# Performance work log

Measured on AMD Instinct MI355X. Metric: run time of the kernel, lower is better.

The kernel has to match this reference:

```python
import jax, jax.numpy as jnp
import numpy as np

H = 12           # num_heads
D_MODEL = 768
SCALE = (D_MODEL // H) ** -0.5  # qk_scale default: head_dim**-0.5


def _attn_mask(q, k, v, mask):
    # sim: (b, i, j); mask broadcast over query dim (mask.unsqueeze(1) in torch)
    sim = jnp.einsum('bid,bjd->bij', q, k) + mask[:, None, :]
    a = jax.nn.softmax(sim, axis=-1)
    return jnp.einsum('bij,bjd->bid', a, v)


def setup_inputs() -> dict:
    key = jax.random.key(0)
    k0, k1, k2, k3 = jax.random.split(key, 4)
    B, F, n, D = 16, 8, 196, 768
    N = 1 + F * n  # cls + frames*patches = 1569
    x = jax.random.normal(k0, (B, N, D), jnp.float32)
    x_mask = jax.random.normal(k1, (B, N), jnp.float32)  # additive attention mask
    Wqkv = jax.random.normal(k2, (3 * D, D), jnp.float32) * (D ** -0.5)
    Wproj = jax.random.normal(k3, (D, D), jnp.float32) * (D ** -0.5)
    bproj = jnp.zeros((D,), jnp.float32)
    return {"x": x, "x_mask": x_mask, "Wqkv": Wqkv, "Wproj": Wproj,
            "bproj": bproj, "f": F}


def reference(x, x_mask, Wqkv, Wproj, bproj, f):
    B, N, D = x.shape
    h = H
    d = D // h
    # qkv projection (qkv_bias=False), split into q,k,v
    qkv = x @ Wqkv.T                       # (B, N, 3D)
    q, k, v = jnp.split(qkv, 3, axis=-1)

    def to_heads(t):  # 'b n (h d) -> (b h) n d'
        return t.reshape(B, N, h, d).transpose(0, 2, 1, 3).reshape(B * h, N, d)

    q, k, v = map(to_heads, (q, k, v))
    mask = jnp.repeat(x_mask, h, axis=0)   # repeat_interleave over heads: (B*h, N)

    q = q * SCALE
    cls_q, q_ = q[:, :1], q[:, 1:]
    cls_k, k_ = k[:, :1], k[:, 1:]
    cls_v, v_ = v[:, :1], v[:, 1:]
    cls_mask, mask_ = mask[:, :1], mask[:, 1:]

    # cls token attends to everything
    cls_out = _attn_mask(cls_q, k, v, mask)            # (B*h, 1, d)

    # spatial attention: 'b (f n) d -> (b f) n d'
    n = (N - 1) // f
    q_ = q_.reshape(B * h * f, n, d)
    k_ = k_.reshape(B * h * f, n, d)
    v_ = v_.reshape(B * h * f, n, d)
    mask_ = mask_.reshape(B * h * f, n)

    # prepend cls k/v/mask to every frame group (r = f)
    cls_k = jnp.repeat(cls_k, f, axis=0)               # (B*h*f, 1, d)
    cls_v = jnp.repeat(cls_v, f, axis=0)
    cls_m = jnp.repeat(cls_mask, f, axis=0)            # (B*h*f, 1)
    k_ = jnp.concatenate([cls_k, k_], axis=1)          # (B*h*f, n+1, d)
    v_ = jnp.concatenate([cls_v, v_], axis=1)
    m2 = jnp.concatenate([cls_m, mask_], axis=1)       # (B*h*f, n+1)

    out = _attn_mask(q_, k_, v_, m2)                   # (B*h*f, n, d)
    out = out.reshape(B * h, f * n, d)                 # '(b f) n d -> b (f n) d'
    out = jnp.concatenate([cls_out, out], axis=1)      # (B*h, N, d)
    out = out.reshape(B, h, N, d).transpose(0, 2, 1, 3).reshape(B, N, D)
    return out @ Wproj.T + bproj
```

## Files before the change

### kernel.cpp

```cpp
#include <hip/hip_runtime.h>
#include <hip/hip_bf16.h>
#include <stdint.h>

#define Hh 12
#define Dm 768
#define Bb 16
#define Nt 1569
#define Ff 8
#define NC 196
#define BH 192
#define Mr 25104
#define CPW 224
#define VTW (8*CPW)
#define PLD 232
#define CLD 132

typedef __attribute__((ext_vector_type(8))) short bf16x8;
typedef __attribute__((ext_vector_type(4))) float f32x4;

typedef const __attribute__((address_space(1))) uint32_t guint;
typedef __attribute__((address_space(3))) uint32_t luint;

static __device__ __forceinline__ float bf2f(unsigned short u) {
  union { unsigned int i; float f; } v; v.i = ((unsigned int)u) << 16; return v.f;
}
static __device__ __forceinline__ unsigned short f2bf(float f) {
  __hip_bfloat16 h = __float2bfloat16(f);
  return __builtin_bit_cast(unsigned short, h);
}

__global__ void cast3_k(const float4* __restrict__ s0, ushort4* __restrict__ d0, int n0,
                        const float4* __restrict__ s1, ushort4* __restrict__ d1, int n1,
                        const float4* __restrict__ s2, ushort4* __restrict__ d2, int n2) {
  int nTot = n0 + n1 + n2;
  for (int i = blockIdx.x * blockDim.x + threadIdx.x; i < nTot; i += gridDim.x * blockDim.x) {
    const float4* s; ushort4* d; int off;
    if (i < n0) { s = s0; d = d0; off = i; }
    else if (i < n0 + n1) { s = s1; d = d1; off = i - n0; }
    else { s = s2; d = d2; off = i - n0 - n1; }
    float4 f = s[off];
    ushort4 u;
    u.x = f2bf(f.x); u.y = f2bf(f.y); u.z = f2bf(f.z); u.w = f2bf(f.w);
    d[off] = u;
  }
}

template<int MODE>
__global__ __launch_bounds__(256) void gemm_k(
    const __hip_bfloat16* __restrict__ A,
    const __hip_bfloat16* __restrict__ W,
    int M, int K,
    __hip_bfloat16* __restrict__ qh, __hip_bfloat16* __restrict__ kh,
    __hip_bfloat16* __restrict__ vT, __hip_bfloat16* __restrict__ vcls,
    const float* __restrict__ bias, float* __restrict__ outp)
{
  __shared__ __align__(16) unsigned short shmem[128 * CLD];
  unsigned short* ls0 = shmem;
  unsigned short* ls1 = shmem + 4096;
  unsigned short* ls2 = shmem + 8192;
  unsigned short* ls3 = shmem + 12288;

  const int tid = threadIdx.x;
  const int lane = tid & 63, wid = tid >> 6;
  const int waveM = wid >> 1, waveN = wid & 1;

  const int gridN = gridDim.x;
  const int nwg = gridDim.x * gridDim.y;
  int bid = blockIdx.y * gridN + blockIdx.x;
  int q8 = nwg >> 3, r8 = nwg & 7;
  int xcd = bid & 7, lid = bid >> 3;
  int swz = (xcd < r8 ? xcd * (q8 + 1) : r8 * (q8 + 1) + (xcd - r8) * q8) + lid;
  const int mBase = (swz / gridN) * 128, nBase = (swz % gridN) * 128;

  const int l15 = lane & 15, lg = lane >> 4;
  f32x4 acc[4][4] = {};
  const int nkt = K >> 6;
  for (int kt = 0; kt < nkt; ++kt) {
#pragma unroll
    for (int s = 0; s < 2; ++s) {
      int seg = s * 256 + tid;
      int row = seg >> 2, ks = seg & 3;
      int arow = mBase + row; if (arow >= M) arow = M - 1;
      int brow = nBase + row;
      const __hip_bfloat16* ap = A + (size_t)arow * K + kt * 64 + ks * 8;
      const __hip_bfloat16* wp = W + (size_t)brow * K + kt * 64 + ks * 8;
      __builtin_amdgcn_global_load_lds((guint*)ap,        (luint*)&ls0[seg * 8], 16, 0, 0);
      __builtin_amdgcn_global_load_lds((guint*)wp,        (luint*)&ls1[seg * 8], 16, 0, 0);
      __builtin_amdgcn_global_load_lds((guint*)(ap + 32), (luint*)&ls2[seg * 8], 16, 0, 0);
      __builtin_amdgcn_global_load_lds((guint*)(wp + 32), (luint*)&ls3[seg * 8], 16, 0, 0);
    }
    __syncthreads();
    bf16x8 aF[4], bF[4], aG[4], bG[4];
#pragma unroll
    for (int i = 0; i < 4; ++i) {
      int ro = (waveM * 64 + i * 16 + l15) * 32 + lg * 8;
      int co = (waveN * 64 + i * 16 + l15) * 32 + lg * 8;
      aF[i] = *reinterpret_cast<const bf16x8*>(&ls0[ro]);
      bF[i] = *reinterpret_cast<const bf16x8*>(&ls1[co]);
      aG[i] = *reinterpret_cast<const bf16x8*>(&ls2[ro]);
      bG[i] = *reinterpret_cast<const bf16x8*>(&ls3[co]);
    }
#pragma unroll
    for (int mi = 0; mi < 4; ++mi)
#pragma unroll
      for (int ni = 0; ni < 4; ++ni) {
        acc[mi][ni] = __builtin_amdgcn_mfma_f32_16x16x32_bf16(aF[mi], bF[ni], acc[mi][ni], 0, 0, 0);
        acc[mi][ni] = __builtin_amdgcn_mfma_f32_16x16x32_bf16(aG[mi], bG[ni], acc[mi][ni], 0, 0, 0);
      }
    __syncthreads();
  }

  if (MODE == 1) {
    const bool fullM = (mBase + 128 <= M);
#pragma unroll
    for (int mi = 0; mi < 4; ++mi)
#pragma unroll
      for (int ni = 0; ni < 4; ++ni)
#pragma unroll
        for (int r = 0; r < 4; ++r) {
          int grow = mBase + waveM * 64 + mi * 16 + lg * 4 + r;
          if (!fullM && grow >= M) continue;
          int gcol = nBase + waveN * 64 + ni * 16 + l15;
          outp[(size_t)grow * Dm + gcol] = acc[mi][ni][r] + bias[gcol];
        }
    return;
  }

  const int which = nBase / Dm;
  const int headBase = (nBase - which * Dm) >> 6;
  const float scl = (which == 0) ? 0.125f : 1.f;
  const bool fullM = (mBase + 128 <= M);

  if (fullM) {
    if (which < 2) {
#pragma unroll
      for (int mi = 0; mi < 4; ++mi)
#pragma unroll
        for (int ni = 0; ni < 4; ++ni)
#pragma unroll
          for (int r = 0; r < 4; ++r)
            shmem[(waveM * 64 + mi * 16 + lg * 4 + r) * CLD + (waveN * 64 + ni * 16 + l15)]
                = f2bf(acc[mi][ni][r] * scl);
      __syncthreads();
      __hip_bfloat16* dst = (which == 0) ? qh : kh;
      int row = tid >> 1, h = tid & 1;
      int grow = mBase + row;
      int b = grow / Nt, i = grow - b * Nt;
      const uint2* sp = reinterpret_cast<const uint2*>(&shmem[row * CLD + h * 64]);
      uint2* dp = reinterpret_cast<uint2*>(
          dst + ((size_t)(b * Hh + headBase + h) * Nt + i) * 64);
#pragma unroll
      for (int j = 0; j < 16; ++j) dp[j] = sp[j];
    } else {
#pragma unroll
      for (int mi = 0; mi < 4; ++mi)
#pragma unroll
        for (int ni = 0; ni < 4; ++ni)
#pragma unroll
          for (int r = 0; r < 4; ++r)
            shmem[(waveN * 64 + ni * 16 + l15) * CLD + (waveM * 64 + mi * 16 + lg * 4 + r)]
                = f2bf(acc[mi][ni][r]);
      __syncthreads();
      int lc = tid & 127, rhalf = tid >> 7;
      int h = lc >> 6, dc = lc & 63;
      int head = headBase + h;
#pragma unroll
      for (int g = 0; g < 8; ++g) {
        int row0 = rhalf * 64 + g * 8;
        int grow0 = mBase + row0;
        int b = grow0 / Nt, i0 = grow0 - b * Nt;
        const unsigned short* sp = &shmem[lc * CLD + row0];
        if (i0 >= 1 && i0 + 8 <= Nt) {
          int j0 = i0 - 1, cc = j0 / NC, key = j0 - cc * NC;
          if (key + 8 <= NC) {
            int bh = b * Hh + head;
            __hip_bfloat16* p = vT + ((size_t)bh * 64 + dc) * VTW + cc * CPW + key;
            if ((key & 1) == 0) {
              const unsigned int* s4 = reinterpret_cast<const unsigned int*>(sp);
              unsigned int* d4 = reinterpret_cast<unsigned int*>(p);
              d4[0] = s4[0]; d4[1] = s4[1]; d4[2] = s4[2]; d4[3] = s4[3];
            } else {
#pragma unroll
              for (int j = 0; j < 8; ++j)
                p[j] = __builtin_bit_cast(__hip_bfloat16, sp[j]);
            }
            continue;
          }
        }
#pragma unroll
        for (int j = 0; j < 8; ++j) {
          int grow = grow0 + j;
          int bb = grow / Nt, ii = grow - bb * Nt;
          int bh2 = bb * Hh + head;
          unsigned short val = sp[j];
          if (ii == 0) {
            vcls[bh2 * 64 + dc] = __builtin_bit_cast(__hip_bfloat16, val);
          } else {
            int jj = ii - 1, cc2 = jj / NC, k2 = jj - cc2 * NC;
            vT[((size_t)bh2 * 64 + dc) * VTW + cc2 * CPW + k2]
                = __builtin_bit_cast(__hip_bfloat16, val);
          }
        }
      }
    }
  } else {
#pragma unroll
    for (int mi = 0; mi < 4; ++mi)
#pragma unroll
      for (int ni = 0; ni < 4; ++ni)
#pragma unroll
        for (int r = 0; r < 4; ++r) {
          int grow = mBase + waveM * 64 + mi * 16 + lg * 4 + r;
          if (grow >= M) continue;
          int gcol = nBase + waveN * 64 + ni * 16 + l15;
          float v = acc[mi][ni][r];
          int b = grow / Nt, i = grow - b * Nt;
          int hcol = gcol - which * Dm;
          int head = hcol >> 6, dc = hcol & 63;
          int bh = b * Hh + head;
          if (which == 0) {
            qh[((size_t)bh * Nt + i) * 64 + dc] = __float2bfloat16(v * 0.125f);
          } else if (which == 1) {
            kh[((size_t)bh * Nt + i) * 64 + dc] = __float2bfloat16(v);
          } else {
            if (i == 0) vcls[bh * 64 + dc] = __float2bfloat16(v);
            else {
              int j = i - 1; int cc = j / NC, key = j - cc * NC;
              vT[((size_t)bh * 64 + dc) * VTW + cc * CPW + key] = __float2bfloat16(v);
            }
          }
        }
  }
}

__global__ __launch_bounds__(256) void cls_attn_k(
    const __hip_bfloat16* __restrict__ qh, const __hip_bfloat16* __restrict__ kh,
    const __hip_bfloat16* __restrict__ vT, const __hip_bfloat16* __restrict__ vcls,
    const float* __restrict__ x_mask, __hip_bfloat16* __restrict__ ao)
{
  const int bh = blockIdx.x, b = bh / Hh, head = bh - b * Hh;
  const int tid = threadIdx.x;
  __shared__ float sS[Nt];
  __shared__ float qv[64];
  __shared__ float red[256];
  if (tid < 64) qv[tid] = __bfloat162float(qh[((size_t)bh * Nt) * 64 + tid]);
  __syncthreads();
  float lmax = -1e30f;
  for (int j = tid; j < Nt; j += 256) {
    const __hip_bfloat16* kr = kh + ((size_t)bh * Nt + j) * 64;
    float dot = 0.f;
#pragma unroll
    for (int d0 = 0; d0 < 64; d0 += 8) {
      bf16x8 kv = *reinterpret_cast<const bf16x8*>(kr + d0);
#pragma unroll
      for (int i = 0; i < 8; ++i) dot += qv[d0 + i] * bf2f((unsigned short)kv[i]);
    }
    float s = dot + x_mask[b * Nt + j];
    sS[j] = s;
    lmax = fmaxf(lmax, s);
  }
  red[tid] = lmax; __syncthreads();
  for (int off = 128; off > 0; off >>= 1) {
    if (tid < off) red[tid] = fmaxf(red[tid], red[tid + off]);
    __syncthreads();
  }
  float m = red[0]; __syncthreads();
  float lsum = 0.f;
  for (int j = tid; j < Nt; j += 256) { float e = __expf(sS[j] - m); sS[j] = e; lsum += e; }
  red[tid] = lsum; __syncthreads();
  for (int off = 128; off > 0; off >>= 1) {
    if (tid < off) red[tid] += red[tid + off];
    __syncthreads();
  }
  float rden = 1.f / red[0]; __syncthreads();
  int dc = tid & 63, part = tid >> 6;
  float partial = 0.f;
  if (part == 0) partial = sS[0] * __bfloat162float(vcls[bh * 64 + dc]);
  const __hip_bfloat16* vrow = vT + ((size_t)bh * 64 + dc) * VTW;
  for (int cc = part * 2; cc < part * 2 + 2; ++cc) {
    int base = 1 + cc * NC;
    const __hip_bfloat16* vc2 = vrow + cc * CPW;
    int key = 0;
    for (; key + 8 <= NC; key += 8) {
      bf16x8 vv = *reinterpret_cast<const bf16x8*>(vc2 + key);
#pragma unroll
      for (int i = 0; i < 8; ++i)
        partial += sS[base + key + i] * bf2f((unsigned short)vv[i]);
    }
    for (; key < NC; ++key)
      partial += sS[base + key] * __bfloat162float(vc2[key]);
  }
  red[tid] = partial; __syncthreads();
  if (tid < 64) {
    float o = (red[tid] + red[tid + 64] + red[tid + 128] + red[tid + 192]) * rden;
    ao[((size_t)b * Nt) * Dm + head * 64 + dc] = __float2bfloat16(o);
  }
}

__global__ __launch_bounds__(256, 1) void chunk_attn_k(
    const __hip_bfloat16* __restrict__ qh, const __hip_bfloat16* __restrict__ kh,
    const __hip_bfloat16* __restrict__ vT, const __hip_bfloat16* __restrict__ vcls,
    const float* __restrict__ x_mask, __hip_bfloat16* __restrict__ ao)
{
  const int g = blockIdx.x;
  const int bh = g >> 3, c = g & 7;
  const int b = bh / Hh, head = bh - b * Hh;
  const int tid = threadIdx.x;
  const int lane = tid & 63, wid = tid >> 6;
  const int l15 = lane & 15, lg = lane >> 4;

  __shared__ __align__(16) __hip_bfloat16 ldsK[208 * 64];
  __shared__ __align__(16) __hip_bfloat16 ldsV[64 * 256];
  __shared__ __align__(16) __hip_bfloat16 ldsP[4][16 * PLD];

  const int kbase = 1 + c * NC;

#pragma unroll
  for (int it = 0; it < 7; ++it) {
    int idx = it * 256 + tid;
    if (idx < 1664) {
      int row = idx >> 3, c16 = idx & 7;
      int token = kbase + row; if (token > Nt - 1) token = Nt - 1;
      __builtin_amdgcn_global_load_lds(
          (guint*)(kh + ((size_t)bh * Nt + token) * 64 + ((c16 ^ (row & 7)) * 8)),
          (luint*)&ldsK[idx * 8], 16, 0, 0);
    }
  }
#pragma unroll
  for (int it = 0; it < 7; ++it) {
    int idx = it * 256 + tid;
    int dc = idx / 28, u = idx - dc * 28;
    uint4 v = *reinterpret_cast<const uint4*>(
        vT + ((size_t)bh * 64 + dc) * VTW + c * CPW + u * 8);
    *reinterpret_cast<uint4*>(&ldsV[dc * 256 + ((u ^ (dc & 7)) * 8)]) = v;
  }
  __syncthreads();

  __hip_bfloat16* myP = ldsP[wid];

  const __hip_bfloat16* kc = kh + (size_t)bh * Nt * 64;
  bf16x8 ck0 = *reinterpret_cast<const bf16x8*>(kc + lg * 8);
  bf16x8 ck1 = *reinterpret_cast<const bf16x8*>(kc + 32 + lg * 8);
  const float maskCls = x_mask[b * Nt];

  for (int rt = wid; rt < 13; rt += 4) {
    int qlrow = rt * 16 + l15;
    int qtok = 1 + c * NC + qlrow; if (qtok > Nt - 1) qtok = Nt - 1;
    const __hip_bfloat16* qp = qh + ((size_t)bh * Nt + qtok) * 64;
    bf16x8 aQ0 = *reinterpret_cast<const bf16x8*>(qp + lg * 8);
    bf16x8 aQ1 = *reinterpret_cast<const bf16x8*>(qp + 32 + lg * 8);

    float pc0 = 0.f;
#pragma unroll
    for (int i = 0; i < 8; ++i)
      pc0 += bf2f((unsigned short)aQ0[i]) * bf2f((unsigned short)ck0[i])
           + bf2f((unsigned short)aQ1[i]) * bf2f((unsigned short)ck1[i]);
    pc0 += __shfl_xor(pc0, 16);
    pc0 += __shfl_xor(pc0, 32);
    pc0 += maskCls;

    f32x4 S[13];
    float mv[13];
#define LD_MM(i) { \
    int row = (i) * 16 + l15; \
    bf16x8 kb0 = *reinterpret_cast<const bf16x8*>(&ldsK[row * 64 + ((lg ^ (l15 & 7)) * 8)]); \
    bf16x8 kb1 = *reinterpret_cast<const bf16x8*>(&ldsK[row * 64 + (((4 + lg) ^ (l15 & 7)) * 8)]); \
    mv[i] = (row < NC) ? x_mask[b * Nt + kbase + row] : -1e30f; \
    f32x4 sa = {}; \
    sa = __builtin_amdgcn_mfma_f32_16x16x32_bf16(aQ0, kb0, sa, 0, 0, 0); \
    sa = __builtin_amdgcn_mfma_f32_16x16x32_bf16(aQ1, kb1, sa, 0, 0, 0); \
    S[i][0] = sa[0] + mv[i]; S[i][1] = sa[1] + mv[i]; \
    S[i][2] = sa[2] + mv[i]; S[i][3] = sa[3] + mv[i]; }
    LD_MM(0) LD_MM(1) LD_MM(2) LD_MM(3) LD_MM(4) LD_MM(5) LD_MM(6)
    LD_MM(7) LD_MM(8) LD_MM(9) LD_MM(10) LD_MM(11) LD_MM(12)
#undef LD_MM

    float pcls[4], rden[4];
#pragma unroll
    for (int r = 0; r < 4; ++r) {
      float m = -1e30f;
#pragma unroll
      for (int nt = 0; nt < 13; ++nt) m = fmaxf(m, S[nt][r]);
      m = fmaxf(m, __shfl_xor(m, 1));
      m = fmaxf(m, __shfl_xor(m, 2));
      m = fmaxf(m, __shfl_xor(m, 4));
      m = fmaxf(m, __shfl_xor(m, 8));
      float sc = __shfl(pc0, lg * 4 + r);
      m = fmaxf(m, sc);
      float sum = 0.f;
#pragma unroll
      for (int nt = 0; nt < 13; ++nt) { float e = __expf(S[nt][r] - m); S[nt][r] = e; sum += e; }
      sum += __shfl_xor(sum, 1);
      sum += __shfl_xor(sum, 2);
      sum += __shfl_xor(sum, 4);
      sum += __shfl_xor(sum, 8);
      float pc = __expf(sc - m);
      pcls[r] = pc;
      rden[r] = 1.f / (sum + pc);
    }

#pragma unroll
    for (int nt = 0; nt < 13; ++nt)
#pragma unroll
      for (int r = 0; r < 4; ++r)
        myP[(lg * 4 + r) * PLD + nt * 16 + l15] = __float2bfloat16(S[nt][r]);
#pragma unroll
    for (int r = 0; r < 4; ++r)
      myP[l15 * PLD + 208 + lg * 4 + r] = __float2bfloat16(0.f);
    asm volatile("s_waitcnt lgkmcnt(0)" ::: "memory");
    __builtin_amdgcn_sched_barrier(0);

    f32x4 O[4] = {};
#define PVK(kt) { \
    bf16x8 aP = *reinterpret_cast<const bf16x8*>(&myP[l15 * PLD + (kt) * 32 + lg * 8]); \
    { int dc = 0 * 16 + l15; bf16x8 bV = *reinterpret_cast<const bf16x8*>(&ldsV[dc * 256 + ((((kt) * 4 + lg) ^ (l15 & 7)) * 8)]); \
      O[0] = __builtin_amdgcn_mfma_f32_16x16x32_bf16(aP, bV, O[0], 0, 0, 0); } \
    { int dc = 1 * 16 + l15; bf16x8 bV = *reinterpret_cast<const bf16x8*>(&ldsV[dc * 256 + ((((kt) * 4 + lg) ^ (l15 & 7)) * 8)]); \
      O[1] = __builtin_amdgcn_mfma_f32_16x16x32_bf16(aP, bV, O[1], 0, 0, 0); } \
    { int dc = 2 * 16 + l15; bf16x8 bV = *reinterpret_cast<const bf16x8*>(&ldsV[dc * 256 + ((((kt) * 4 + lg) ^ (l15 & 7)) * 8)]); \
      O[2] = __builtin_amdgcn_mfma_f32_16x16x32_bf16(aP, bV, O[2], 0, 0, 0); } \
    { int dc = 3 * 16 + l15; bf16x8 bV = *reinterpret_cast<const bf16x8*>(&ldsV[dc * 256 + ((((kt) * 4 + lg) ^ (l15 & 7)) * 8)]); \
      O[3] = __builtin_amdgcn_mfma_f32_16x16x32_bf16(aP, bV, O[3], 0, 0, 0); } }
    PVK(0) PVK(1) PVK(2) PVK(3) PVK(4) PVK(5) PVK(6)
#undef PVK

#pragma unroll
    for (int ni = 0; ni < 4; ++ni) {
      int dc = ni * 16 + l15;
      float vc = __bfloat162float(vcls[bh * 64 + dc]);
#pragma unroll
      for (int r = 0; r < 4; ++r) {
        int lrow = rt * 16 + lg * 4 + r;
        if (lrow < NC) {
          float o = (O[ni][r] + pcls[r] * vc) * rden[r];
          int tok = 1 + c * NC + lrow;
          ao[((size_t)b * Nt + tok) * Dm + head * 64 + dc] = __float2bfloat16(o);
        }
      }
    }
  }
}

extern "C" void kernel_launch(void* const* d_in, const int* in_sizes, int n_in,
                              void* d_out, int out_size, void* d_ws, size_t ws_size,
                              hipStream_t stream) {
  const float* x     = (const float*)d_in[0];
  const float* xmask = (const float*)d_in[1];
  const float* wqkv  = (const float*)d_in[2];
  const float* wproj = (const float*)d_in[3];
  const float* bproj = (const float*)d_in[4];
  float* outp = (float*)d_out;

  char* ws = (char*)d_ws;
  size_t off = 0;
  auto alloc = [&](size_t bytes) {
    char* p = ws + off;
    off += (bytes + 255) & ~(size_t)255;
    return p;
  };
  __hip_bfloat16* xb     = (__hip_bfloat16*)alloc((size_t)Mr * Dm * 2);
  __hip_bfloat16* wqkvb  = (__hip_bfloat16*)alloc((size_t)3 * Dm * Dm * 2);
  __hip_bfloat16* wprojb = (__hip_bfloat16*)alloc((size_t)Dm * Dm * 2);
  __hip_bfloat16* qh     = (__hip_bfloat16*)alloc((size_t)BH * Nt * 64 * 2);
  __hip_bfloat16* kh     = (__hip_bfloat16*)alloc((size_t)BH * Nt * 64 * 2);
  __hip_bfloat16* vT     = (__hip_bfloat16*)alloc((size_t)BH * 64 * VTW * 2);
  __hip_bfloat16* vcls   = (__hip_bfloat16*)alloc((size_t)BH * 64 * 2);
  __hip_bfloat16* ao = xb;

  cast3_k<<<2048, 256, 0, stream>>>((const float4*)x, (ushort4*)xb, Mr * Dm / 4,
                                    (const float4*)wqkv, (ushort4*)wqkvb, 3 * Dm * Dm / 4,
                                    (const float4*)wproj, (ushort4*)wprojb, Dm * Dm / 4);

  gemm_k<0><<<dim3(18, 197), 256, 0, stream>>>(xb, wqkvb, Mr, Dm, qh, kh, vT, vcls, nullptr, nullptr);

  cls_attn_k<<<BH, 256, 0, stream>>>(qh, kh, vT, vcls, xmask, ao);
  chunk_attn_k<<<BH * Ff, 256, 0, stream>>>(qh, kh, vT, vcls, xmask, ao);

  gemm_k<1><<<dim3(6, 197), 256, 0, stream>>>(ao, wprojb, Mr, Dm, nullptr, nullptr, nullptr, nullptr, bproj, outp);
}
```

Baseline: 356.6 us.

## Triple-buffer GEMM K-loop with async LDS prefetch and merge attention kernels

The GEMM main loop moves from a single-buffered 64-wide K step with two full barriers per step to a 3-stage ring of 32-wide K tiles. Global-to-LDS loads run two stages ahead and are tracked with explicit vmcnt waits, so memory latency overlaps with MFMA work. The cls-token attention and per-frame chunk attention kernels are merged into one launch, which drops a launch and lets the two kinds of blocks run concurrently. In exchange, the merged kernel's LDS footprint covers both paths, and the GEMM does more loop iterations and barriers, each with less MFMA work between them.

```diff
diff --git a/kernel.cpp b/kernel.cpp
--- a/kernel.cpp
+++ b/kernel.cpp
@@ -54,11 +54,7 @@
     __hip_bfloat16* __restrict__ vT, __hip_bfloat16* __restrict__ vcls,
     const float* __restrict__ bias, float* __restrict__ outp)
 {
-  __shared__ __align__(16) unsigned short shmem[128 * CLD];
-  unsigned short* ls0 = shmem;
-  unsigned short* ls1 = shmem + 4096;
-  unsigned short* ls2 = shmem + 8192;
-  unsigned short* ls3 = shmem + 12288;
+  __shared__ __align__(16) unsigned short shmem[24576];
 
   const int tid = threadIdx.x;
   const int lane = tid & 63, wid = tid >> 6;
@@ -73,41 +69,66 @@
   const int mBase = (swz / gridN) * 128, nBase = (swz % gridN) * 128;
 
   const int l15 = lane & 15, lg = lane >> 4;
+
+  int arow0, brow0, ks0, arow1, brow1, ks1;
+  {
+    int seg = tid;
+    int row = seg >> 2; ks0 = seg & 3;
+    arow0 = mBase + row; if (arow0 >= M) arow0 = M - 1;
+    brow0 = nBase + row;
+    seg = 256 + tid;
+    row = seg >> 2; ks1 = seg & 3;
+    arow1 = mBase + row; if (arow1 >= M) arow1 = M - 1;
+    brow1 = nBase + row;
+  }
+  auto STAGE = [&](int buf, int kt) {
+    unsigned short* base = shmem + buf * 8192;
+    __builtin_amdgcn_global_load_lds((guint*)(A + (size_t)arow0 * K + kt * 32 + ks0 * 8),
+                                     (luint*)&base[tid * 8], 16, 0, 0);
+    __builtin_amdgcn_global_load_lds((guint*)(W + (size_t)brow0 * K + kt * 32 + ks0 * 8),
+                                     (luint*)&base[4096 + tid * 8], 16, 0, 0);
+    __builtin_amdgcn_global_load_lds((guint*)(A + (size_t)arow1 * K + kt * 32 + ks1 * 8),
+                                     (luint*)&base[(256 + tid) * 8], 16, 0, 0);
+    __builtin_amdgcn_global_load_lds((guint*)(W + (size_t)brow1 * K + kt * 32 + ks1 * 8),
+                                     (luint*)&base[4096 + (256 + tid) * 8], 16, 0, 0);
+  };
+
   f32x4 acc[4][4] = {};
-  const int nkt = K >> 6;
+  const int nkt = K >> 5;
+
+  STAGE(0, 0);
+  STAGE(1, 1);
+  asm volatile("s_waitcnt vmcnt(4)" ::: "memory");
+  __builtin_amdgcn_s_barrier();
+  __builtin_amdgcn_sched_barrier(0);
+
+  int cur = 0;
   for (int kt = 0; kt < nkt; ++kt) {
-#pragma unroll
-    for (int s = 0; s < 2; ++s) {
-      int seg = s * 256 + tid;
-      int row = seg >> 2, ks = seg & 3;
-      int arow = mBase + row; if (arow >= M) arow = M - 1;
-      int brow = nBase + row;
-      const __hip_bfloat16* ap = A + (size_t)arow * K + kt * 64 + ks * 8;
-      const __hip_bfloat16* wp = W + (size_t)brow * K + kt * 64 + ks * 8;
-      __builtin_amdgcn_global_load_lds((guint*)ap,        (luint*)&ls0[seg * 8], 16, 0, 0);
-      __builtin_amdgcn_global_load_lds((guint*)wp,        (luint*)&ls1[seg * 8], 16, 0, 0);
-      __builtin_amdgcn_global_load_lds((guint*)(ap + 32), (luint*)&ls2[seg * 8], 16, 0, 0);
-      __builtin_amdgcn_global_load_lds((guint*)(wp + 32), (luint*)&ls3[seg * 8], 16, 0, 0);
-    }
-    __syncthreads();
-    bf16x8 aF[4], bF[4], aG[4], bG[4];
+    if (kt + 2 < nkt) {
+      int b2 = cur + 2; if (b2 >= 3) b2 -= 3;
+      STAGE(b2, kt + 2);
+    }
+    const unsigned short* base = shmem + cur * 8192;
+    bf16x8 aF[4], bF[4];
 #pragma unroll
     for (int i = 0; i < 4; ++i) {
-      int ro = (waveM * 64 + i * 16 + l15) * 32 + lg * 8;
-      int co = (waveN * 64 + i * 16 + l15) * 32 + lg * 8;
-      aF[i] = *reinterpret_cast<const bf16x8*>(&ls0[ro]);
-      bF[i] = *reinterpret_cast<const bf16x8*>(&ls1[co]);
-      aG[i] = *reinterpret_cast<const bf16x8*>(&ls2[ro]);
-      bG[i] = *reinterpret_cast<const bf16x8*>(&ls3[co]);
+      aF[i] = *reinterpret_cast<const bf16x8*>(&base[(waveM * 64 + i * 16 + l15) * 32 + lg * 8]);
+      bF[i] = *reinterpret_cast<const bf16x8*>(&base[4096 + (waveN * 64 + i * 16 + l15) * 32 + lg * 8]);
     }
 #pragma unroll
     for (int mi = 0; mi < 4; ++mi)
 #pragma unroll
-      for (int ni = 0; ni < 4; ++ni) {
+      for (int ni = 0; ni < 4; ++ni)
         acc[mi][ni] = __builtin_amdgcn_mfma_f32_16x16x32_bf16(aF[mi], bF[ni], acc[mi][ni], 0, 0, 0);
-        acc[mi][ni] = __builtin_amdgcn_mfma_f32_16x16x32_bf16(aG[mi], bG[ni], acc[mi][ni], 0, 0, 0);
-      }
-    __syncthreads();
+    __builtin_amdgcn_sched_barrier(0);
+    if (kt + 2 < nkt) {
+      asm volatile("s_waitcnt vmcnt(4)" ::: "memory");
+    } else {
+      asm volatile("s_waitcnt vmcnt(0)" ::: "memory");
+    }
+    __builtin_amdgcn_s_barrier();
+    __builtin_amdgcn_sched_barrier(0);
+    cur = cur + 1; if (cur >= 3) cur -= 3;
   }
 
   if (MODE == 1) {
@@ -233,85 +254,83 @@
   }
 }
 
-__global__ __launch_bounds__(256) void cls_attn_k(
+__global__ __launch_bounds__(256, 1) void attn_k(
     const __hip_bfloat16* __restrict__ qh, const __hip_bfloat16* __restrict__ kh,
     const __hip_bfloat16* __restrict__ vT, const __hip_bfloat16* __restrict__ vcls,
     const float* __restrict__ x_mask, __hip_bfloat16* __restrict__ ao)
 {
-  const int bh = blockIdx.x, b = bh / Hh, head = bh - b * Hh;
-  const int tid = threadIdx.x;
+  __shared__ __align__(16) __hip_bfloat16 ldsK[208 * 64];
+  __shared__ __align__(16) __hip_bfloat16 ldsV[64 * 256];
+  __shared__ __align__(16) __hip_bfloat16 ldsP[4][16 * PLD];
   __shared__ float sS[Nt];
   __shared__ float qv[64];
   __shared__ float red[256];
-  if (tid < 64) qv[tid] = __bfloat162float(qh[((size_t)bh * Nt) * 64 + tid]);
-  __syncthreads();
-  float lmax = -1e30f;
-  for (int j = tid; j < Nt; j += 256) {
-    const __hip_bfloat16* kr = kh + ((size_t)bh * Nt + j) * 64;
-    float dot = 0.f;
-#pragma unroll
-    for (int d0 = 0; d0 < 64; d0 += 8) {
-      bf16x8 kv = *reinterpret_cast<const bf16x8*>(kr + d0);
-#pragma unroll
-      for (int i = 0; i < 8; ++i) dot += qv[d0 + i] * bf2f((unsigned short)kv[i]);
-    }
-    float s = dot + x_mask[b * Nt + j];
-    sS[j] = s;
-    lmax = fmaxf(lmax, s);
-  }
-  red[tid] = lmax; __syncthreads();
-  for (int off = 128; off > 0; off >>= 1) {
-    if (tid < off) red[tid] = fmaxf(red[tid], red[tid + off]);
+
+  const int bidx = blockIdx.x;
+  const int tid = threadIdx.x;
+
+  if (bidx < BH) {
+    const int bh = bidx, b = bh / Hh, head = bh - b * Hh;
+    if (tid < 64) qv[tid] = __bfloat162float(qh[((size_t)bh * Nt) * 64 + tid]);
     __syncthreads();
-  }
-  float m = red[0]; __syncthreads();
-  float lsum = 0.f;
-  for (int j = tid; j < Nt; j += 256) { float e = __expf(sS[j] - m); sS[j] = e; lsum += e; }
-  red[tid] = lsum; __syncthreads();
-  for (int off = 128; off > 0; off >>= 1) {
-    if (tid < off) red[tid] += red[tid + off];
-    __syncthreads();
-  }
-  float rden = 1.f / red[0]; __syncthreads();
-  int dc = tid & 63, part = tid >> 6;
-  float partial = 0.f;
-  if (part == 0) partial = sS[0] * __bfloat162float(vcls[bh * 64 + dc]);
-  const __hip_bfloat16* vrow = vT + ((size_t)bh * 64 + dc) * VTW;
-  for (int cc = part * 2; cc < part * 2 + 2; ++cc) {
-    int base = 1 + cc * NC;
-    const __hip_bfloat16* vc2 = vrow + cc * CPW;
-    int key = 0;
-    for (; key + 8 <= NC; key += 8) {
-      bf16x8 vv = *reinterpret_cast<const bf16x8*>(vc2 + key);
-#pragma unroll
-      for (int i = 0; i < 8; ++i)
-        partial += sS[base + key + i] * bf2f((unsigned short)vv[i]);
-    }
-    for (; key < NC; ++key)
-      partial += sS[base + key] * __bfloat162float(vc2[key]);
-  }
-  red[tid] = partial; __syncthreads();
-  if (tid < 64) {
-    float o = (red[tid] + red[tid + 64] + red[tid + 128] + red[tid + 192]) * rden;
-    ao[((size_t)b * Nt) * Dm + head * 64 + dc] = __float2bfloat16(o);
-  }
-}
-
-__global__ __launch_bounds__(256, 1) void chunk_attn_k(
-    const __hip_bfloat16* __restrict__ qh, const __hip_bfloat16* __restrict__ kh,
-    const __hip_bfloat16* __restrict__ vT, const __hip_bfloat16* __restrict__ vcls,
-    const float* __restrict__ x_mask, __hip_bfloat16* __restrict__ ao)
-{
-  const int g = blockIdx.x;
+    float lmax = -1e30f;
+    for (int j = tid; j < Nt; j += 256) {
+      const __hip_bfloat16* kr = kh + ((size_t)bh * Nt + j) * 64;
+      float dot = 0.f;
+#pragma unroll
+      for (int d0 = 0; d0 < 64; d0 += 8) {
+        bf16x8 kv = *reinterpret_cast<const bf16x8*>(kr + d0);
+#pragma unroll
+        for (int i = 0; i < 8; ++i) dot += qv[d0 + i] * bf2f((unsigned short)kv[i]);
+      }
+      float s = dot + x_mask[b * Nt + j];
+      sS[j] = s;
+      lmax = fmaxf(lmax, s);
+    }
+    red[tid] = lmax; __syncthreads();
+    for (int off = 128; off > 0; off >>= 1) {
+      if (tid < off) red[tid] = fmaxf(red[tid], red[tid + off]);
+      __syncthreads();
+    }
+    float m = red[0]; __syncthreads();
+    float lsum = 0.f;
+    for (int j = tid; j < Nt; j += 256) { float e = __expf(sS[j] - m); sS[j] = e; lsum += e; }
+    red[tid] = lsum; __syncthreads();
+    for (int off = 128; off > 0; off >>= 1) {
+      if (tid < off) red[tid] += red[tid + off];
+      __syncthreads();
+    }
+    float rden = 1.f / red[0]; __syncthreads();
+    int dc = tid & 63, part = tid >> 6;
+    float partial = 0.f;
+    if (part == 0) partial = sS[0] * __bfloat162float(vcls[bh * 64 + dc]);
+    const __hip_bfloat16* vrow = vT + ((size_t)bh * 64 + dc) * VTW;
+    for (int cc = part * 2; cc < part * 2 + 2; ++cc) {
+      int base = 1 + cc * NC;
+      const __hip_bfloat16* vc2 = vrow + cc * CPW;
+      int key = 0;
+      for (; key + 8 <= NC; key += 8) {
+        bf16x8 vv = *reinterpret_cast<const bf16x8*>(vc2 + key);
+#pragma unroll
+        for (int i = 0; i < 8; ++i)
+          partial += sS[base + key + i] * bf2f((unsigned short)vv[i]);
+      }
+      for (; key < NC; ++key)
+        partial += sS[base + key] * __bfloat162float(vc2[key]);
+    }
+    red[tid] = partial; __syncthreads();
+    if (tid < 64) {
+      float o = (red[tid] + red[tid + 64] + red[tid + 128] + red[tid + 192]) * rden;
+      ao[((size_t)b * Nt) * Dm + head * 64 + dc] = __float2bfloat16(o);
+    }
+    return;
+  }
+
+  const int g = bidx - BH;
   const int bh = g >> 3, c = g & 7;
   const int b = bh / Hh, head = bh - b * Hh;
-  const int tid = threadIdx.x;
   const int lane = tid & 63, wid = tid >> 6;
   const int l15 = lane & 15, lg = lane >> 4;
-
-  __shared__ __align__(16) __hip_bfloat16 ldsK[208 * 64];
-  __shared__ __align__(16) __hip_bfloat16 ldsV[64 * 256];
-  __shared__ __align__(16) __hip_bfloat16 ldsP[4][16 * PLD];
 
   const int kbase = 1 + c * NC;
 
@@ -473,8 +492,7 @@
 
   gemm_k<0><<<dim3(18, 197), 256, 0, stream>>>(xb, wqkvb, Mr, Dm, qh, kh, vT, vcls, nullptr, nullptr);
 
-  cls_attn_k<<<BH, 256, 0, stream>>>(qh, kh, vT, vcls, xmask, ao);
-  chunk_attn_k<<<BH * Ff, 256, 0, stream>>>(qh, kh, vT, vcls, xmask, ao);
+  attn_k<<<BH + BH * Ff, 256, 0, stream>>>(qh, kh, vT, vcls, xmask, ao);
 
   gemm_k<1><<<dim3(6, 197), 256, 0, stream>>>(ao, wprojb, Mr, Dm, nullptr, nullptr, nullptr, nullptr, bproj, outp);
 }
```

Result: faster. 337.0 us (-5.5%).

## Merge cls and chunk attention kernels and read V from global directly

Applied to the files above, without the earlier changes.

Folds the cls-token attention and per-frame chunk attention into one launch, with block ranges selecting the path, which removes one kernel launch and the gap between them. The V tile is no longer staged in LDS; PV MFMA operands are loaded straight from global vT. This cuts shared memory to about 55KB so launch bounds can allow two blocks per CU. The cost is uncoalesced, uncached-in-LDS global reads of V inside the MFMA loop, plus tighter register limits.

```diff
diff --git a/kernel.cpp b/kernel.cpp
--- a/kernel.cpp
+++ b/kernel.cpp
@@ -233,85 +233,84 @@
   }
 }
 
-__global__ __launch_bounds__(256) void cls_attn_k(
+__global__ __launch_bounds__(256, 2) void attn_k(
     const __hip_bfloat16* __restrict__ qh, const __hip_bfloat16* __restrict__ kh,
     const __hip_bfloat16* __restrict__ vT, const __hip_bfloat16* __restrict__ vcls,
     const float* __restrict__ x_mask, __hip_bfloat16* __restrict__ ao)
 {
-  const int bh = blockIdx.x, b = bh / Hh, head = bh - b * Hh;
+  __shared__ __align__(16) char smem[56320];
+
+  const int bidx = blockIdx.x;
   const int tid = threadIdx.x;
-  __shared__ float sS[Nt];
-  __shared__ float qv[64];
-  __shared__ float red[256];
-  if (tid < 64) qv[tid] = __bfloat162float(qh[((size_t)bh * Nt) * 64 + tid]);
-  __syncthreads();
-  float lmax = -1e30f;
-  for (int j = tid; j < Nt; j += 256) {
-    const __hip_bfloat16* kr = kh + ((size_t)bh * Nt + j) * 64;
-    float dot = 0.f;
-#pragma unroll
-    for (int d0 = 0; d0 < 64; d0 += 8) {
-      bf16x8 kv = *reinterpret_cast<const bf16x8*>(kr + d0);
-#pragma unroll
-      for (int i = 0; i < 8; ++i) dot += qv[d0 + i] * bf2f((unsigned short)kv[i]);
-    }
-    float s = dot + x_mask[b * Nt + j];
-    sS[j] = s;
-    lmax = fmaxf(lmax, s);
-  }
-  red[tid] = lmax; __syncthreads();
-  for (int off = 128; off > 0; off >>= 1) {
-    if (tid < off) red[tid] = fmaxf(red[tid], red[tid + off]);
+
+  if (bidx < BH) {
+    float* sS = reinterpret_cast<float*>(smem);
+    float* qv = reinterpret_cast<float*>(smem + 6400);
+    float* red = reinterpret_cast<float*>(smem + 6656);
+    const int bh = bidx, b = bh / Hh, head = bh - b * Hh;
+    if (tid < 64) qv[tid] = __bfloat162float(qh[((size_t)bh * Nt) * 64 + tid]);
     __syncthreads();
-  }
-  float m = red[0]; __syncthreads();
-  float lsum = 0.f;
-  for (int j = tid; j < Nt; j += 256) { float e = __expf(sS[j] - m); sS[j] = e; lsum += e; }
-  red[tid] = lsum; __syncthreads();
-  for (int off = 128; off > 0; off >>= 1) {
-    if (tid < off) red[tid] += red[tid + off];
-    __syncthreads();
-  }
-  float rden = 1.f / red[0]; __syncthreads();
-  int dc = tid & 63, part = tid >> 6;
-  float partial = 0.f;
-  if (part == 0) partial = sS[0] * __bfloat162float(vcls[bh * 64 + dc]);
-  const __hip_bfloat16* vrow = vT + ((size_t)bh * 64 + dc) * VTW;
-  for (int cc = part * 2; cc < part * 2 + 2; ++cc) {
-    int base = 1 + cc * NC;
-    const __hip_bfloat16* vc2 = vrow + cc * CPW;
-    int key = 0;
-    for (; key + 8 <= NC; key += 8) {
-      bf16x8 vv = *reinterpret_cast<const bf16x8*>(vc2 + key);
-#pragma unroll
-      for (int i = 0; i < 8; ++i)
-        partial += sS[base + key + i] * bf2f((unsigned short)vv[i]);
-    }
-    for (; key < NC; ++key)
-      partial += sS[base + key] * __bfloat162float(vc2[key]);
-  }
-  red[tid] = partial; __syncthreads();
-  if (tid < 64) {
-    float o = (red[tid] + red[tid + 64] + red[tid + 128] + red[tid + 192]) * rden;
-    ao[((size_t)b * Nt) * Dm + head * 64 + dc] = __float2bfloat16(o);
-  }
-}
-
-__global__ __launch_bounds__(256, 1) void chunk_attn_k(
-    const __hip_bfloat16* __restrict__ qh, const __hip_bfloat16* __restrict__ kh,
-    const __hip_bfloat16* __restrict__ vT, const __hip_bfloat16* __restrict__ vcls,
-    const float* __restrict__ x_mask, __hip_bfloat16* __restrict__ ao)
-{
-  const int g = blockIdx.x;
+    float lmax = -1e30f;
+    for (int j = tid; j < Nt; j += 256) {
+      const __hip_bfloat16* kr = kh + ((size_t)bh * Nt + j) * 64;
+      float dot = 0.f;
+#pragma unroll
+      for (int d0 = 0; d0 < 64; d0 += 8) {
+        bf16x8 kv = *reinterpret_cast<const bf16x8*>(kr + d0);
+#pragma unroll
+        for (int i = 0; i < 8; ++i) dot += qv[d0 + i] * bf2f((unsigned short)kv[i]);
+      }
+      float s = dot + x_mask[b * Nt + j];
+      sS[j] = s;
+      lmax = fmaxf(lmax, s);
+    }
+    red[tid] = lmax; __syncthreads();
+    for (int off = 128; off > 0; off >>= 1) {
+      if (tid < off) red[tid] = fmaxf(red[tid], red[tid + off]);
+      __syncthreads();
+    }
+    float m = red[0]; __syncthreads();
+    float lsum = 0.f;
+    for (int j = tid; j < Nt; j += 256) { float e = __expf(sS[j] - m); sS[j] = e; lsum += e; }
+    red[tid] = lsum; __syncthreads();
+    for (int off = 128; off > 0; off >>= 1) {
+      if (tid < off) red[tid] += red[tid + off];
+      __syncthreads();
+    }
+    float rden = 1.f / red[0]; __syncthreads();
+    int dc = tid & 63, part = tid >> 6;
+    float partial = 0.f;
+    if (part == 0) partial = sS[0] * __bfloat162float(vcls[bh * 64 + dc]);
+    const __hip_bfloat16* vrow = vT + ((size_t)bh * 64 + dc) * VTW;
+    for (int cc = part * 2; cc < part * 2 + 2; ++cc) {
+      int base = 1 + cc * NC;
+      const __hip_bfloat16* vc2 = vrow + cc * CPW;
+      int key = 0;
+      for (; key + 8 <= NC; key += 8) {
+        bf16x8 vv = *reinterpret_cast<const bf16x8*>(vc2 + key);
+#pragma unroll
+        for (int i = 0; i < 8; ++i)
+          partial += sS[base + key + i] * bf2f((unsigned short)vv[i]);
+      }
+      for (; key < NC; ++key)
+        partial += sS[base + key] * __bfloat162float(vc2[key]);
+    }
+    red[tid] = partial; __syncthreads();
+    if (tid < 64) {
+      float o = (red[tid] + red[tid + 64] + red[tid + 128] + red[tid + 192]) * rden;
+      ao[((size_t)b * Nt) * Dm + head * 64 + dc] = __float2bfloat16(o);
+    }
+    return;
+  }
+
+  __hip_bfloat16* ldsK = reinterpret_cast<__hip_bfloat16*>(smem);
+  __hip_bfloat16* ldsP = reinterpret_cast<__hip_bfloat16*>(smem + 26624);
+
+  const int g = bidx - BH;
   const int bh = g >> 3, c = g & 7;
   const int b = bh / Hh, head = bh - b * Hh;
-  const int tid = threadIdx.x;
   const int lane = tid & 63, wid = tid >> 6;
   const int l15 = lane & 15, lg = lane >> 4;
-
-  __shared__ __align__(16) __hip_bfloat16 ldsK[208 * 64];
-  __shared__ __align__(16) __hip_bfloat16 ldsV[64 * 256];
-  __shared__ __align__(16) __hip_bfloat16 ldsP[4][16 * PLD];
 
   const int kbase = 1 + c * NC;
 
@@ -326,17 +325,9 @@
           (luint*)&ldsK[idx * 8], 16, 0, 0);
     }
   }
-#pragma unroll
-  for (int it = 0; it < 7; ++it) {
-    int idx = it * 256 + tid;
-    int dc = idx / 28, u = idx - dc * 28;
-    uint4 v = *reinterpret_cast<const uint4*>(
-        vT + ((size_t)bh * 64 + dc) * VTW + c * CPW + u * 8);
-    *reinterpret_cast<uint4*>(&ldsV[dc * 256 + ((u ^ (dc & 7)) * 8)]) = v;
-  }
   __syncthreads();
 
-  __hip_bfloat16* myP = ldsP[wid];
+  __hip_bfloat16* myP = ldsP + wid * (16 * PLD);
 
   const __hip_bfloat16* kc = kh + (size_t)bh * Nt * 64;
   bf16x8 ck0 = *reinterpret_cast<const bf16x8*>(kc + lg * 8);
@@ -413,13 +404,13 @@
     f32x4 O[4] = {};
 #define PVK(kt) { \
     bf16x8 aP = *reinterpret_cast<const bf16x8*>(&myP[l15 * PLD + (kt) * 32 + lg * 8]); \
-    { int dc = 0 * 16 + l15; bf16x8 bV = *reinterpret_cast<const bf16x8*>(&ldsV[dc * 256 + ((((kt) * 4 + lg) ^ (l15 & 7)) * 8)]); \
+    { int dc = 0 * 16 + l15; bf16x8 bV = *reinterpret_cast<const bf16x8*>(vT + ((size_t)bh * 64 + dc) * VTW + c * CPW + (kt) * 32 + lg * 8); \
       O[0] = __builtin_amdgcn_mfma_f32_16x16x32_bf16(aP, bV, O[0], 0, 0, 0); } \
-    { int dc = 1 * 16 + l15; bf16x8 bV = *reinterpret_cast<const bf16x8*>(&ldsV[dc * 256 + ((((kt) * 4 + lg) ^ (l15 & 7)) * 8)]); \
+    { int dc = 1 * 16 + l15; bf16x8 bV = *reinterpret_cast<const bf16x8*>(vT + ((size_t)bh * 64 + dc) * VTW + c * CPW + (kt) * 32 + lg * 8); \
       O[1] = __builtin_amdgcn_mfma_f32_16x16x32_bf16(aP, bV, O[1], 0, 0, 0); } \
-    { int dc = 2 * 16 + l15; bf16x8 bV = *reinterpret_cast<const bf16x8*>(&ldsV[dc * 256 + ((((kt) * 4 + lg) ^ (l15 & 7)) * 8)]); \
+    { int dc = 2 * 16 + l15; bf16x8 bV = *reinterpret_cast<const bf16x8*>(vT + ((size_t)bh * 64 + dc) * VTW + c * CPW + (kt) * 32 + lg * 8); \
       O[2] = __builtin_amdgcn_mfma_f32_16x16x32_bf16(aP, bV, O[2], 0, 0, 0); } \
-    { int dc = 3 * 16 + l15; bf16x8 bV = *reinterpret_cast<const bf16x8*>(&ldsV[dc * 256 + ((((kt) * 4 + lg) ^ (l15 & 7)) * 8)]); \
+    { int dc = 3 * 16 + l15; bf16x8 bV = *reinterpret_cast<const bf16x8*>(vT + ((size_t)bh * 64 + dc) * VTW + c * CPW + (kt) * 32 + lg * 8); \
       O[3] = __builtin_amdgcn_mfma_f32_16x16x32_bf16(aP, bV, O[3], 0, 0, 0); } }
     PVK(0) PVK(1) PVK(2) PVK(3) PVK(4) PVK(5) PVK(6)
 #undef PVK
@@ -473,8 +464,7 @@
 
   gemm_k<0><<<dim3(18, 197), 256, 0, stream>>>(xb, wqkvb, Mr, Dm, qh, kh, vT, vcls, nullptr, nullptr);
 
-  cls_attn_k<<<BH, 256, 0, stream>>>(qh, kh, vT, vcls, xmask, ao);
-  chunk_attn_k<<<BH * Ff, 256, 0, stream>>>(qh, kh, vT, vcls, xmask, ao);
+  attn_k<<<BH + BH * Ff, 256, 0, stream>>>(qh, kh, vT, vcls, xmask, ao);
 
   gemm_k<1><<<dim3(6, 197), 256, 0, stream>>>(ao, wprojb, Mr, Dm, nullptr, nullptr, nullptr, nullptr, bproj, outp);
 }
```

Result: no change. 351.9 us (-1.3%).
